# Optimization experiments

Hardware: AMD Instinct MI355X
Metric: run time of the kernel (lower is better)

## Reference

```python
import jax, jax.numpy as jnp
import numpy as np

N_NODES = 50000
N_EDGES = 800000
HID = 256
OUT = 128
NEG_SLOPE = 0.2


def gat_layer(x, src, dst, W_src, W_dst, a_src_vec, a_dst_vec, bias, n_nodes):
    # Dense projections (PyG lin_src / lin_dst for tuple in_channels)
    h_src = x @ W_src              # [N, C]
    h_dst = x @ W_dst              # [N, C]
    # Per-node attention logits (att_src/att_dst dot products)
    a_src = h_src @ a_src_vec      # [N]
    a_dst = h_dst @ a_dst_vec      # [N]
    # Edge logits + LeakyReLU
    e = jax.nn.leaky_relu(a_src[src] + a_dst[dst], NEG_SLOPE)  # [E]
    # Segment softmax over incoming edges of each dst node
    m = jax.ops.segment_max(e, dst, num_segments=n_nodes)      # [N]
    m = jnp.where(jnp.isfinite(m), m, 0.0)                      # empty segments
    ex = jnp.exp(e - m[dst])                                    # [E]
    s = jax.ops.segment_sum(ex, dst, num_segments=n_nodes)     # [N]
    alpha = ex / (s[dst] + 1e-16)                               # [E]
    # Attention-weighted message aggregation (scatter-add to dst)
    msg = alpha[:, None] * h_src[src]                           # [E, C]
    out = jax.ops.segment_sum(msg, dst, num_segments=n_nodes)  # [N, C]
    return out + bias


def setup_inputs() -> dict:
    key = jax.random.key(0)
    ks = jax.random.split(key, 12)
    x = jax.random.normal(ks[0], (N_NODES, HID), dtype=jnp.float32)
    edge_index = jax.random.randint(ks[1], (2, N_EDGES), 0, N_NODES, dtype=jnp.int64)
    sc1 = 1.0 / np.sqrt(HID)
    sc2 = 1.0 / np.sqrt(HID)
    return {
        "x": x,
        "edge_index": edge_index,
        "W1_src": jax.random.normal(ks[2], (HID, HID), dtype=jnp.float32) * sc1,
        "W1_dst": jax.random.normal(ks[3], (HID, HID), dtype=jnp.float32) * sc1,
        "att1_src": jax.random.normal(ks[4], (HID,), dtype=jnp.float32) * sc1,
        "att1_dst": jax.random.normal(ks[5], (HID,), dtype=jnp.float32) * sc1,
        "b1": jnp.zeros((HID,), dtype=jnp.float32),
        "W2_src": jax.random.normal(ks[6], (HID, OUT), dtype=jnp.float32) * sc2,
        "W2_dst": jax.random.normal(ks[7], (HID, OUT), dtype=jnp.float32) * sc2,
        "att2_src": jax.random.normal(ks[8], (OUT,), dtype=jnp.float32) * (1.0 / np.sqrt(OUT)),
        "att2_dst": jax.random.normal(ks[9], (OUT,), dtype=jnp.float32) * (1.0 / np.sqrt(OUT)),
        "b2": jnp.zeros((OUT,), dtype=jnp.float32),
    }


def reference(x, edge_index, W1_src, W1_dst, att1_src, att1_dst, b1,
              W2_src, W2_dst, att2_src, att2_dst, b2):
    src, dst = edge_index[0], edge_index[1]
    h = gat_layer(x, src, dst, W1_src, W1_dst, att1_src, att1_dst, b1, N_NODES)
    h = jax.nn.relu(h)
    out = gat_layer(h, src, dst, W2_src, W2_dst, att2_src, att2_dst, b2, N_NODES)
    return out
```

## Files before the change

kernel.cpp:

```cpp
#include <hip/hip_runtime.h>
#include <math.h>

#define N_NODES 50000
#define N_EDGES 800000
#define HID 256
#define OUT_C 128
#define NEG_SLOPE 0.2f
#define SCAN_NB ((N_NODES + 255) / 256)

typedef __attribute__((ext_vector_type(8))) short bf16x8;
typedef __attribute__((ext_vector_type(4))) float f32x4;
typedef _Float16 half_t;
typedef __attribute__((ext_vector_type(4))) _Float16 half4;
typedef __attribute__((ext_vector_type(2))) _Float16 half2t;

__device__ inline unsigned short bf16_rne(float x) {
    unsigned u = __float_as_uint(x);
    return (unsigned short)((u + 0x7fffu + ((u >> 16) & 1u)) >> 16);
}

__device__ __forceinline__ void async_copy16(const void* g, void* l) {
    __builtin_amdgcn_global_load_lds(
        (const __attribute__((address_space(1))) unsigned int*)g,
        (__attribute__((address_space(3))) unsigned int*)l, 16, 0, 0);
}

#define PACK1_T (8 * 17 * 64)
#define PACK2_T (8 * 9 * 64)
#define EDGE_BLOCKS ((N_EDGES + 255) / 256)
#define PACK_BLOCKS ((PACK1_T + PACK2_T + 255) / 256)
#define V_BLOCKS 128


__global__ __launch_bounds__(256) void hist_prep_kernel(
    const int* __restrict__ dst, int* __restrict__ counts, int* __restrict__ rank,
    const float* __restrict__ W1s, const float* __restrict__ att1s,
    const float* __restrict__ W1d, const float* __restrict__ att1d,
    const float* __restrict__ W2s, const float* __restrict__ att2s,
    const float* __restrict__ W2d, const float* __restrict__ att2d,
    unsigned short* __restrict__ hi1, unsigned short* __restrict__ lo1,
    unsigned short* __restrict__ hi2, unsigned short* __restrict__ lo2) {
    if (blockIdx.x < EDGE_BLOCKS) {
        int e = blockIdx.x * 256 + threadIdx.x;
        if (e < N_EDGES) rank[e] = atomicAdd(&counts[dst[e]], 1);
        return;
    }
    if (blockIdx.x < EDGE_BLOCKS + PACK_BLOCKS) {
        int t = (blockIdx.x - EDGE_BLOCKS) * 256 + threadIdx.x;
        const float *W; unsigned short *hi, *lo; int cout, NTL, tt;
        if (t < PACK1_T)            { tt = t;           W = W1s; hi = hi1; lo = lo1; cout = HID;  NTL = 17; }
        else if (t < PACK1_T + PACK2_T) { tt = t - PACK1_T; W = W2s; hi = hi2; lo = lo2; cout = OUT_C; NTL = 9; }
        else return;
        int lane = tt & 63;
        int tile = (tt >> 6) % NTL;
        if (tile == NTL - 1) return;
        int ks = tt / (64 * NTL);
        int m = lane & 15;
        int kbase = ks * 32 + (lane >> 4) * 8;
        #pragma unroll
        for (int j = 0; j < 8; j++) {
            float val = W[(size_t)(kbase + j) * cout + tile * 16 + m];
            unsigned short h = bf16_rne(val);
            hi[tt * 8 + j] = h;
            lo[tt * 8 + j] = bf16_rne(val - __uint_as_float((unsigned)h << 16));
        }
        return;
    }
    int vb = blockIdx.x - EDGE_BLOCKS - PACK_BLOCKS;
    int layer = vb >> 6;
    int wave = threadIdx.x >> 6, lane = threadIdx.x & 63;
    int k = (vb & 63) * 4 + wave;
    const float *Ws, *Wd, *as_, *ad_; unsigned short *hi, *lo; int cout, NTL;
    if (layer == 0) { Ws = W1s; Wd = W1d; as_ = att1s; ad_ = att1d; hi = hi1; lo = lo1; cout = HID;  NTL = 17; }
    else            { Ws = W2s; Wd = W2d; as_ = att2s; ad_ = att2d; hi = hi2; lo = lo2; cout = OUT_C; NTL = 9; }
    float vs = 0.f, vd = 0.f;
    for (int j = lane; j < cout; j += 64) {
        vs += Ws[(size_t)k * cout + j] * as_[j];
        vd += Wd[(size_t)k * cout + j] * ad_[j];
    }
    #pragma unroll
    for (int off = 32; off > 0; off >>= 1) {
        vs += __shfl_down(vs, off);
        vd += __shfl_down(vd, off);
    }
    vs = __shfl(vs, 0);
    vd = __shfl(vd, 0);
    int ks = k >> 5, quad = (k >> 3) & 3, j = k & 7;
    if (lane < 32) {
        int m = lane & 15;
        int tt = ks * 64 * NTL + (NTL - 1) * 64 + quad * 16 + m;
        float val = (m == 0) ? vs : (m == 1) ? vd : 0.f;
        unsigned short h = bf16_rne(val);
        if (lane < 16) hi[tt * 8 + j] = h;
        else           lo[tt * 8 + j] = bf16_rne(val - __uint_as_float((unsigned)h << 16));
    }
}


__global__ __launch_bounds__(256) void block_scan_kernel(
    const int* __restrict__ counts, int* __restrict__ excl,
    int* __restrict__ blockSums, int n) {
    __shared__ int waveSums[4];
    int i = blockIdx.x * 256 + threadIdx.x;
    int lane = threadIdx.x & 63;
    int wv = threadIdx.x >> 6;
    int c = (i < n) ? counts[i] : 0;
    int v = c;
    #pragma unroll
    for (int off = 1; off < 64; off <<= 1) {
        int t = __shfl_up(v, off);
        if (lane >= off) v += t;
    }
    if (lane == 63) waveSums[wv] = v;
    __syncthreads();
    int waveOff = 0;
    #pragma unroll
    for (int w = 0; w < 4; w++)
        if (w < wv) waveOff += waveSums[w];
    if (i < n) excl[i] = waveOff + v - c;
    if (threadIdx.x == 255) blockSums[blockIdx.x] = waveOff + v;
}

__global__ __launch_bounds__(256) void add_offsets_kernel(
    int* __restrict__ excl, const int* __restrict__ blockSums, int n) {
    __shared__ int lds[4];
    int tid = threadIdx.x;
    int partial = 0;
    for (int j = tid; j < (int)blockIdx.x; j += 256) partial += blockSums[j];
    #pragma unroll
    for (int off = 32; off > 0; off >>= 1) partial += __shfl_down(partial, off);
    if ((tid & 63) == 0) lds[tid >> 6] = partial;
    __syncthreads();
    int prefix = lds[0] + lds[1] + lds[2] + lds[3];
    int i = blockIdx.x * 256 + tid;
    if (i < n) excl[i] += prefix;
    if (i == 0) excl[n] = N_EDGES;
}

__global__ __launch_bounds__(256) void scatter_kernel(
    const int* __restrict__ src, const int* __restrict__ dst,
    const int* __restrict__ offsets, const int* __restrict__ rank,
    int* __restrict__ src_sorted) {
    int e = blockIdx.x * 256 + threadIdx.x;
    if (e >= N_EDGES) return;
    src_sorted[offsets[dst[e]] + rank[e]] = src[e];
}


template <int COUT, int NT, int RG, bool WRITE_A, bool ASPLIT>
__device__ __forceinline__ void gemm_body(
    const float* __restrict__ A,
    const unsigned short* __restrict__ Ahi, const unsigned short* __restrict__ Alo,
    const unsigned short* __restrict__ Bhi, const unsigned short* __restrict__ Blo,
    half_t* __restrict__ H,
    float* __restrict__ a_s, float* __restrict__ a_d, int M, int tile0,
    short* sBh, short* sBl) {
    const int NTL = COUT / 16 + 1;
    int wave = threadIdx.x >> 6, lane = threadIdx.x & 63;
    int m = lane & 15, quad = lane >> 4;
    int row0 = blockIdx.x * (RG * 64) + wave * (RG * 16);
    f32x4 acc[RG][NT];
    #pragma unroll
    for (int rg = 0; rg < RG; rg++)
        #pragma unroll
        for (int nt = 0; nt < NT; nt++)
            acc[rg][nt] = (f32x4){0.f, 0.f, 0.f, 0.f};

    const float* arow[RG];
    const unsigned short* arh[RG];
    const unsigned short* arl[RG];
    #pragma unroll
    for (int rg = 0; rg < RG; rg++) {
        int r = row0 + rg * 16 + m;
        if (r >= M) r = M - 1;
        if (ASPLIT) {
            arh[rg] = Ahi + (size_t)r * HID;
            arl[rg] = Alo + (size_t)r * HID;
        } else {
            arow[rg] = A + (size_t)r * HID;
        }
    }

    auto STAGE = [&](int ks, int b) {
        for (int u = wave; u < 2 * NT; u += 4) {
            int nt = (u < NT) ? u : u - NT;
            int tile = (WRITE_A && nt == NT - 1) ? (COUT / 16) : (tile0 + nt);
            size_t goff = ((size_t)(ks * NTL + tile) * 64 + lane) * 8;
            if (u < NT) async_copy16(Bhi + goff, sBh + b * NT * 512 + nt * 512);
            else        async_copy16(Blo + goff, sBl + b * NT * 512 + nt * 512);
        }
    };

    bf16x8 ahc[RG], alc[RG];
    #pragma unroll
    for (int rg = 0; rg < RG; rg++) {
        if (ASPLIT) {
            ahc[rg] = *(const bf16x8*)(arh[rg] + quad * 8);
            alc[rg] = *(const bf16x8*)(arl[rg] + quad * 8);
        } else {
            const float* ap = arow[rg] + quad * 8;
            float4 v0 = *(const float4*)ap;
            float4 v1 = *(const float4*)(ap + 4);
            float av[8] = {v0.x, v0.y, v0.z, v0.w, v1.x, v1.y, v1.z, v1.w};
            #pragma unroll
            for (int j = 0; j < 8; j++) {
                unsigned short h = bf16_rne(av[j]);
                ahc[rg][j] = (short)h;
                alc[rg][j] = (short)bf16_rne(av[j] - __uint_as_float((unsigned)h << 16));
            }
        }
    }

    STAGE(0, 0);
    __syncthreads();
    int cur = 0;
    for (int ks = 0; ks < 8; ks++) {
        float4 a0n[RG], a1n[RG];
        bf16x8 ahn[RG], aln[RG];
        if (ks < 7) {
            STAGE(ks + 1, cur ^ 1);
            #pragma unroll
            for (int rg = 0; rg < RG; rg++) {
                if (ASPLIT) {
                    ahn[rg] = *(const bf16x8*)(arh[rg] + (ks + 1) * 32 + quad * 8);
                    aln[rg] = *(const bf16x8*)(arl[rg] + (ks + 1) * 32 + quad * 8);
                } else {
                    const float* ap = arow[rg] + (ks + 1) * 32 + quad * 8;
                    a0n[rg] = *(const float4*)ap;
                    a1n[rg] = *(const float4*)(ap + 4);
                }
            }
        }
        #pragma unroll
        for (int nt = 0; nt < NT; nt++) {
            bf16x8 bh = *(const bf16x8*)(sBh + cur * NT * 512 + nt * 512 + lane * 8);
            bf16x8 bl = *(const bf16x8*)(sBl + cur * NT * 512 + nt * 512 + lane * 8);
            #pragma unroll
            for (int rg = 0; rg < RG; rg++) {
                acc[rg][nt] = __builtin_amdgcn_mfma_f32_16x16x32_bf16(ahc[rg], bh, acc[rg][nt], 0, 0, 0);
                acc[rg][nt] = __builtin_amdgcn_mfma_f32_16x16x32_bf16(ahc[rg], bl, acc[rg][nt], 0, 0, 0);
                acc[rg][nt] = __builtin_amdgcn_mfma_f32_16x16x32_bf16(alc[rg], bh, acc[rg][nt], 0, 0, 0);
            }
        }
        if (ks < 7) {
            #pragma unroll
            for (int rg = 0; rg < RG; rg++) {
                if (ASPLIT) {
                    ahc[rg] = ahn[rg];
                    alc[rg] = aln[rg];
                } else {
                    float av[8] = {a0n[rg].x, a0n[rg].y, a0n[rg].z, a0n[rg].w,
                                   a1n[rg].x, a1n[rg].y, a1n[rg].z, a1n[rg].w};
                    #pragma unroll
                    for (int j = 0; j < 8; j++) {
                        unsigned short h = bf16_rne(av[j]);
                        ahc[rg][j] = (short)h;
                        alc[rg][j] = (short)bf16_rne(av[j] - __uint_as_float((unsigned)h << 16));
                    }
                }
            }
        }
        __syncthreads();
        cur ^= 1;
    }
    const int NW = WRITE_A ? NT - 1 : NT;
    #pragma unroll
    for (int rg = 0; rg < RG; rg++)
        #pragma unroll
        for (int nt = 0; nt < NW; nt++)
            #pragma unroll
            for (int r = 0; r < 4; r++) {
                int row = row0 + rg * 16 + quad * 4 + r;
                if (row < M)
                    H[(size_t)row * COUT + (tile0 + nt) * 16 + m] = (half_t)acc[rg][nt][r];
            }
    if (WRITE_A) {
        #pragma unroll
        for (int rg = 0; rg < RG; rg++)
            #pragma unroll
            for (int r = 0; r < 4; r++) {
                int row = row0 + rg * 16 + quad * 4 + r;
                if (row < M) {
                    if (m == 0) a_s[row] = acc[rg][NT - 1][r];
                    else if (m == 1) a_d[row] = acc[rg][NT - 1][r];
                }
            }
    }
}

template <int COUT, int RG, bool ASPLIT>
__global__ __launch_bounds__(256) void mfma_gemm_a_kernel(
    const float* __restrict__ A,
    const unsigned short* __restrict__ Ahi, const unsigned short* __restrict__ Alo,
    const unsigned short* __restrict__ Bhi, const unsigned short* __restrict__ Blo,
    half_t* __restrict__ H,
    float* __restrict__ a_s, float* __restrict__ a_d, int M) {
    __shared__ short sBh[2 * 9 * 512];
    __shared__ short sBl[2 * 9 * 512];
    if (blockIdx.y == 0)
        gemm_body<COUT, 9, RG, true, ASPLIT>(A, Ahi, Alo, Bhi, Blo, H, a_s, a_d, M, 0, sBh, sBl);
    else
        gemm_body<COUT, 8, RG, false, ASPLIT>(A, Ahi, Alo, Bhi, Blo, H, a_s, a_d, M, 8, sBh, sBl);
}


template <int C, bool RELU, bool OSPLIT>
__global__ __launch_bounds__(256) void fused_aggregate_kernel(
    const int* __restrict__ offsets, const int* __restrict__ src_sorted,
    const float* __restrict__ a_src, const float* __restrict__ a_dst,
    const half_t* __restrict__ h, const float* __restrict__ bias,
    float* __restrict__ out,
    unsigned short* __restrict__ outhi, unsigned short* __restrict__ outlo) {
    constexpr int CH = 8;
    int node = (int)((blockIdx.x * 256u + threadIdx.x) >> 6);
    int lane = threadIdx.x & 63;
    if (node >= N_NODES) return;
    int beg = offsets[node], end = offsets[node + 1];
    float ad = a_dst[node];
    float s = 0.f;

    if (C == 256) {
        float4 acc = make_float4(0.f, 0.f, 0.f, 0.f);
        for (int base = beg; base < end; base += CH) {
            int cnt = end - base; if (cnt > CH) cnt = CH;
            int idx[CH];
            #pragma unroll
            for (int j = 0; j < CH; j++)
                idx[j] = src_sorted[(j < cnt) ? base + j : base];
            half4 hv[CH];
            #pragma unroll
            for (int j = 0; j < CH; j++)
                hv[j] = *(const half4*)(h + ((unsigned)idx[j] * C + lane * 4));
            float w[CH];
            #pragma unroll
            for (int j = 0; j < CH; j++) {
                float l = a_src[idx[j]] + ad;
                l = fmaxf(l, l * NEG_SLOPE);
                w[j] = (j < cnt) ? __expf(l) : 0.f;
                s += w[j];
            }
            #pragma unroll
            for (int j = 0; j < CH; j++) {
                acc.x += w[j] * (float)hv[j][0]; acc.y += w[j] * (float)hv[j][1];
                acc.z += w[j] * (float)hv[j][2]; acc.w += w[j] * (float)hv[j][3];
            }
        }
        float inv = 1.f / (s + 1e-16f);
        float4 bv = *(const float4*)(bias + lane * 4);
        acc.x = acc.x * inv + bv.x; acc.y = acc.y * inv + bv.y;
        acc.z = acc.z * inv + bv.z; acc.w = acc.w * inv + bv.w;
        if (RELU) {
            acc.x = fmaxf(acc.x, 0.f); acc.y = fmaxf(acc.y, 0.f);
            acc.z = fmaxf(acc.z, 0.f); acc.w = fmaxf(acc.w, 0.f);
        }
        if (OSPLIT) {
            float o[4] = {acc.x, acc.y, acc.z, acc.w};
            ushort4 h4, l4;
            unsigned short* hp = (unsigned short*)&h4;
            unsigned short* lp = (unsigned short*)&l4;
            #pragma unroll
            for (int j = 0; j < 4; j++) {
                unsigned short hh = bf16_rne(o[j]);
                hp[j] = hh;
                lp[j] = bf16_rne(o[j] - __uint_as_float((unsigned)hh << 16));
            }
            *(ushort4*)(outhi + (size_t)node * C + lane * 4) = h4;
            *(ushort4*)(outlo + (size_t)node * C + lane * 4) = l4;
        } else {
            *(float4*)(out + (size_t)node * C + lane * 4) = acc;
        }
    } else {
        float2 acc = make_float2(0.f, 0.f);
        for (int base = beg; base < end; base += CH) {
            int cnt = end - base; if (cnt > CH) cnt = CH;
            int idx[CH];
            #pragma unroll
            for (int j = 0; j < CH; j++)
                idx[j] = src_sorted[(j < cnt) ? base + j : base];
            half2t hv[CH];
            #pragma unroll
            for (int j = 0; j < CH; j++)
                hv[j] = *(const half2t*)(h + ((unsigned)idx[j] * C + lane * 2));
            float w[CH];
            #pragma unroll
            for (int j = 0; j < CH; j++) {
                float l = a_src[idx[j]] + ad;
                l = fmaxf(l, l * NEG_SLOPE);
                w[j] = (j < cnt) ? __expf(l) : 0.f;
                s += w[j];
            }
            #pragma unroll
            for (int j = 0; j < CH; j++) {
                acc.x += w[j] * (float)hv[j][0]; acc.y += w[j] * (float)hv[j][1];
            }
        }
        float inv = 1.f / (s + 1e-16f);
        float2 bv = *(const float2*)(bias + lane * 2);
        acc.x = acc.x * inv + bv.x; acc.y = acc.y * inv + bv.y;
        if (RELU) { acc.x = fmaxf(acc.x, 0.f); acc.y = fmaxf(acc.y, 0.f); }
        *(float2*)(out + (size_t)node * C + lane * 2) = acc;
    }
}

extern "C" void kernel_launch(void* const* d_in, const int* in_sizes, int n_in,
                              void* d_out, int out_size, void* d_ws, size_t ws_size,
                              hipStream_t stream) {
    const float* x     = (const float*)d_in[0];
    const int*   edge  = (const int*)d_in[1];
    const int*   src   = edge;
    const int*   dst   = edge + N_EDGES;
    const float* W1s   = (const float*)d_in[2];
    const float* W1d   = (const float*)d_in[3];
    const float* att1s = (const float*)d_in[4];
    const float* att1d = (const float*)d_in[5];
    const float* b1    = (const float*)d_in[6];
    const float* W2s   = (const float*)d_in[7];
    const float* W2d   = (const float*)d_in[8];
    const float* att2s = (const float*)d_in[9];
    const float* att2d = (const float*)d_in[10];
    const float* b2    = (const float*)d_in[11];
    float* out = (float*)d_out;

    float* ws    = (float*)d_ws;
    half_t* h1   = (half_t*)ws;
    unsigned short* act2hi = (unsigned short*)(ws + (size_t)N_NODES * HID);
    unsigned short* act2lo = act2hi + (size_t)N_NODES * HID;
    float* a_s   = ws + 2 * (size_t)N_NODES * HID;
    float* a_d   = a_s + N_NODES;
    int* ibase      = (int*)(a_d + N_NODES);
    int* src_sorted = ibase;
    int* rank       = src_sorted + N_EDGES;
    int* counts     = rank + N_EDGES;
    int* offsets    = counts + N_NODES;
    int* blockSums  = offsets + N_NODES + 1;
    unsigned short* wp1h = (unsigned short*)(((uintptr_t)(blockSums + SCAN_NB) + 15) & ~(uintptr_t)15);
    unsigned short* wp1l = wp1h + PACK1_T * 8;
    unsigned short* wp2h = wp1l + PACK1_T * 8;
    unsigned short* wp2l = wp2h + PACK2_T * 8;
    half_t* h2 = h1;

    const int waveBlocksN = (N_NODES + 3) / 4;
    const int gemmBlocks1 = (N_NODES + 127) / 128;
    const int gemmBlocks2 = (N_NODES + 63) / 64;

    hipMemsetAsync(counts, 0, N_NODES * sizeof(int), stream);
    hist_prep_kernel<<<EDGE_BLOCKS + PACK_BLOCKS + V_BLOCKS, 256, 0, stream>>>(
        dst, counts, rank,
        W1s, att1s, W1d, att1d, W2s, att2s, W2d, att2d,
        wp1h, wp1l, wp2h, wp2l);
    block_scan_kernel<<<SCAN_NB, 256, 0, stream>>>(counts, offsets, blockSums, N_NODES);
    add_offsets_kernel<<<SCAN_NB, 256, 0, stream>>>(offsets, blockSums, N_NODES);
    scatter_kernel<<<EDGE_BLOCKS, 256, 0, stream>>>(src, dst, offsets, rank, src_sorted);

    mfma_gemm_a_kernel<HID, 2, false><<<dim3(gemmBlocks1, 2), 256, 0, stream>>>(
        x, nullptr, nullptr, wp1h, wp1l, h1, a_s, a_d, N_NODES);
    fused_aggregate_kernel<HID, true, true><<<waveBlocksN, 256, 0, stream>>>(
        offsets, src_sorted, a_s, a_d, h1, b1, nullptr, act2hi, act2lo);

    mfma_gemm_a_kernel<OUT_C, 1, true><<<dim3(gemmBlocks2, 1), 256, 0, stream>>>(
        nullptr, act2hi, act2lo, wp2h, wp2l, h2, a_s, a_d, N_NODES);
    fused_aggregate_kernel<OUT_C, false, false><<<waveBlocksN, 256, 0, stream>>>(
        offsets, src_sorted, a_s, a_d, h2, b2, out, nullptr, nullptr);
}
```

Baseline: 305.5 us.

## Fuse edge scatter into layer-1 GEMM launch and split aggregation into halves

The CSR scatter of source indices now runs as extra blocks appended to the layer-1 GEMM grid, removing one kernel launch and letting the scatter overlap with GEMM blocks. The layer-1 aggregation is split into two launches, each covering half the nodes. The split adds a launch and has no clear benefit, so it may be an experiment. The scatter blocks along blockIdx.y=1 return immediately, which wastes some launched blocks.

```diff
diff --git a/kernel.cpp b/kernel.cpp
--- a/kernel.cpp
+++ b/kernel.cpp
@@ -137,15 +137,6 @@
     if (i == 0) excl[n] = N_EDGES;
 }
 
-__global__ __launch_bounds__(256) void scatter_kernel(
-    const int* __restrict__ src, const int* __restrict__ dst,
-    const int* __restrict__ offsets, const int* __restrict__ rank,
-    int* __restrict__ src_sorted) {
-    int e = blockIdx.x * 256 + threadIdx.x;
-    if (e >= N_EDGES) return;
-    src_sorted[offsets[dst[e]] + rank[e]] = src[e];
-}
-
 
 template <int COUT, int NT, int RG, bool WRITE_A, bool ASPLIT>
 __device__ __forceinline__ void gemm_body(
@@ -288,15 +279,26 @@
     }
 }
 
-template <int COUT, int RG, bool ASPLIT>
+template <int COUT, int RG, bool ASPLIT, bool SCATTER>
 __global__ __launch_bounds__(256) void mfma_gemm_a_kernel(
     const float* __restrict__ A,
     const unsigned short* __restrict__ Ahi, const unsigned short* __restrict__ Alo,
     const unsigned short* __restrict__ Bhi, const unsigned short* __restrict__ Blo,
     half_t* __restrict__ H,
-    float* __restrict__ a_s, float* __restrict__ a_d, int M) {
+    float* __restrict__ a_s, float* __restrict__ a_d, int M, int gemmNB,
+    const int* __restrict__ src, const int* __restrict__ dst,
+    const int* __restrict__ offsets, const int* __restrict__ rank,
+    int* __restrict__ src_sorted) {
     __shared__ short sBh[2 * 9 * 512];
     __shared__ short sBl[2 * 9 * 512];
+    if (SCATTER && (int)blockIdx.x >= gemmNB) {
+        if (blockIdx.y == 0) {
+            int e = ((int)blockIdx.x - gemmNB) * 256 + threadIdx.x;
+            if (e < N_EDGES)
+                src_sorted[offsets[dst[e]] + rank[e]] = src[e];
+        }
+        return;
+    }
     if (blockIdx.y == 0)
         gemm_body<COUT, 9, RG, true, ASPLIT>(A, Ahi, Alo, Bhi, Blo, H, a_s, a_d, M, 0, sBh, sBl);
     else
@@ -310,11 +312,12 @@
     const float* __restrict__ a_src, const float* __restrict__ a_dst,
     const half_t* __restrict__ h, const float* __restrict__ bias,
     float* __restrict__ out,
-    unsigned short* __restrict__ outhi, unsigned short* __restrict__ outlo) {
+    unsigned short* __restrict__ outhi, unsigned short* __restrict__ outlo,
+    int node0, int nodeEnd) {
     constexpr int CH = 8;
-    int node = (int)((blockIdx.x * 256u + threadIdx.x) >> 6);
+    int node = node0 + (int)((blockIdx.x * 256u + threadIdx.x) >> 6);
     int lane = threadIdx.x & 63;
-    if (node >= N_NODES) return;
+    if (node >= nodeEnd) return;
     int beg = offsets[node], end = offsets[node + 1];
     float ad = a_dst[node];
     float s = 0.f;
@@ -439,9 +442,11 @@
     unsigned short* wp2l = wp2h + PACK2_T * 8;
     half_t* h2 = h1;
 
-    const int waveBlocksN = (N_NODES + 3) / 4;
     const int gemmBlocks1 = (N_NODES + 127) / 128;
     const int gemmBlocks2 = (N_NODES + 63) / 64;
+    const int NHALF = N_NODES / 2;
+    const int aggHalfBlocks = (NHALF + 3) / 4;
+    const int waveBlocksN = (N_NODES + 3) / 4;
 
     hipMemsetAsync(counts, 0, N_NODES * sizeof(int), stream);
     hist_prep_kernel<<<EDGE_BLOCKS + PACK_BLOCKS + V_BLOCKS, 256, 0, stream>>>(
@@ -450,15 +455,20 @@
         wp1h, wp1l, wp2h, wp2l);
     block_scan_kernel<<<SCAN_NB, 256, 0, stream>>>(counts, offsets, blockSums, N_NODES);
     add_offsets_kernel<<<SCAN_NB, 256, 0, stream>>>(offsets, blockSums, N_NODES);
-    scatter_kernel<<<EDGE_BLOCKS, 256, 0, stream>>>(src, dst, offsets, rank, src_sorted);
-
-    mfma_gemm_a_kernel<HID, 2, false><<<dim3(gemmBlocks1, 2), 256, 0, stream>>>(
-        x, nullptr, nullptr, wp1h, wp1l, h1, a_s, a_d, N_NODES);
-    fused_aggregate_kernel<HID, true, true><<<waveBlocksN, 256, 0, stream>>>(
-        offsets, src_sorted, a_s, a_d, h1, b1, nullptr, act2hi, act2lo);
-
-    mfma_gemm_a_kernel<OUT_C, 1, true><<<dim3(gemmBlocks2, 1), 256, 0, stream>>>(
-        nullptr, act2hi, act2lo, wp2h, wp2l, h2, a_s, a_d, N_NODES);
+
+    mfma_gemm_a_kernel<HID, 2, false, true>
+        <<<dim3(gemmBlocks1 + EDGE_BLOCKS, 2), 256, 0, stream>>>(
+        x, nullptr, nullptr, wp1h, wp1l, h1, a_s, a_d, N_NODES, gemmBlocks1,
+        src, dst, offsets, rank, src_sorted);
+    fused_aggregate_kernel<HID, true, true><<<aggHalfBlocks, 256, 0, stream>>>(
+        offsets, src_sorted, a_s, a_d, h1, b1, nullptr, act2hi, act2lo, 0, NHALF);
+    fused_aggregate_kernel<HID, true, true><<<aggHalfBlocks, 256, 0, stream>>>(
+        offsets, src_sorted, a_s, a_d, h1, b1, nullptr, act2hi, act2lo, NHALF, N_NODES);
+
+    mfma_gemm_a_kernel<OUT_C, 1, true, false>
+        <<<dim3(gemmBlocks2, 1), 256, 0, stream>>>(
+        nullptr, act2hi, act2lo, wp2h, wp2l, h2, a_s, a_d, N_NODES, gemmBlocks2,
+        nullptr, nullptr, nullptr, nullptr, nullptr);
     fused_aggregate_kernel<OUT_C, false, false><<<waveBlocksN, 256, 0, stream>>>(
-        offsets, src_sorted, a_s, a_d, h2, b2, out, nullptr, nullptr);
-}
+        offsets, src_sorted, a_s, a_d, h2, b2, out, nullptr, nullptr, 0, N_NODES);
+}
```

After: 314.2 us. +2.9%, slower.
